# Kernel optimization log

Hardware: AMD Instinct MI355X
Metric: run time of the kernel (lower is better)

The kernel has to match this reference:

```python
import jax, jax.numpy as jnp
import numpy as np

B, T, H, W = 4, 32, 160, 320
NF, FPF = 8, 8          # num_filters, features_per_filter
SPEED_DIM = 8           # speed_embedding output width
U = 64                  # internal LTC neurons (wiring units)
S = NF * FPF + SPEED_DIM  # 72 sensory inputs
M = 1                   # motor (output) neurons
ODE_UNFOLDS = 6
EPS = 1e-8


def setup_inputs() -> dict:
    key = jax.random.key(0)
    k = jax.random.split(key, 20)
    f32 = jnp.float32
    sp = (H // 8) * (W // 8)  # spatial size per filter after 3 stride-2 convs = 800
    d = {}
    d["input_sequence"] = jax.random.normal(k[0], (B, T, 3, H, W), f32)
    d["speed_sequence"] = jax.random.uniform(k[1], (B, T, 1), f32)
    # conv head params
    d["conv1_w"] = jax.random.normal(k[2], (16, 3, 5, 5), f32) * 0.05
    d["conv1_b"] = jnp.zeros((16,), f32)
    d["conv2_w"] = jax.random.normal(k[3], (32, 16, 5, 5), f32) * 0.05
    d["conv2_b"] = jnp.zeros((32,), f32)
    d["conv3_w"] = jax.random.normal(k[4], (NF, 32, 5, 5), f32) * 0.05
    d["conv3_b"] = jnp.zeros((NF,), f32)
    d["head_w"] = jax.random.normal(k[5], (NF, sp, FPF), f32) * 0.02  # per-filter Linear
    d["head_b"] = jnp.zeros((NF, FPF), f32)
    # speed embedding MLP (Dropout is identity at inference)
    d["se_w1"] = jax.random.normal(k[6], (1, 16), f32) * 0.5
    d["se_b1"] = jnp.zeros((16,), f32)
    d["se_w2"] = jax.random.normal(k[7], (16, SPEED_DIM), f32) * 0.3
    d["se_b2"] = jnp.zeros((SPEED_DIM,), f32)
    # LTC cell params (ncps-style init ranges)
    d["input_w"] = jnp.ones((S,), f32)
    d["input_b"] = jnp.zeros((S,), f32)
    d["gleak"] = jax.random.uniform(k[8], (U,), f32, 0.001, 1.0)
    d["vleak"] = jax.random.uniform(k[9], (U,), f32, -0.2, 0.2)
    d["cm"] = jax.random.uniform(k[10], (U,), f32, 0.4, 0.6)
    d["sigma"] = jax.random.uniform(k[11], (U, U), f32, 3.0, 8.0)
    d["mu"] = jax.random.uniform(k[12], (U, U), f32, 0.3, 0.8)
    d["w_syn"] = jax.random.uniform(k[13], (U, U), f32, 0.001, 1.0)
    d["erev"] = jnp.asarray(jax.random.bernoulli(k[14], 0.5, (U, U)), f32) * 2.0 - 1.0
    d["sensory_sigma"] = jax.random.uniform(k[15], (S, U), f32, 3.0, 8.0)
    d["sensory_mu"] = jax.random.uniform(k[16], (S, U), f32, 0.3, 0.8)
    d["sensory_w"] = jax.random.uniform(k[17], (S, U), f32, 0.001, 1.0)
    d["sensory_erev"] = jnp.asarray(jax.random.bernoulli(k[18], 0.5, (S, U)), f32) * 2.0 - 1.0
    d["output_w"] = jnp.ones((M,), f32)
    d["output_b"] = jnp.zeros((M,), f32)
    return d


def _conv(x, w, b, stride):
    y = jax.lax.conv_general_dilated(
        x, w, (stride, stride), [(2, 2), (2, 2)],
        dimension_numbers=("NCHW", "OIHW", "NCHW"))
    return jax.nn.relu(y + b[None, :, None, None])


def reference(input_sequence, speed_sequence, conv1_w, conv1_b, conv2_w, conv2_b,
              conv3_w, conv3_b, head_w, head_b, se_w1, se_b1, se_w2, se_b2,
              input_w, input_b, gleak, vleak, cm, sigma, mu, w_syn, erev,
              sensory_sigma, sensory_mu, sensory_w, sensory_erev, output_w, output_b):
    Bv, Tv = input_sequence.shape[:2]
    # ---- conv head over all frames at once ----
    x = input_sequence.reshape(Bv * Tv, 3, H, W)
    x = _conv(x, conv1_w, conv1_b, 2)
    x = _conv(x, conv2_w, conv2_b, 2)
    x = _conv(x, conv3_w, conv3_b, 2)          # [N, NF, H/8, W/8]
    x = x.reshape(Bv * Tv, NF, -1)             # [N, NF, 800]
    feats = jnp.einsum("nfp,fpk->nfk", x, head_w) + head_b  # per-filter Linear
    feats = feats.reshape(Bv, Tv, NF * FPF)    # [B, T, 64]
    # global-std normalization (torch .std() uses ddof=1)
    feats = feats / (jnp.std(feats, ddof=1) + 1e-5)
    # ---- speed embedding (vectorized over B,T) ----
    s = speed_sequence[..., :1]                # [B, T, 1]
    emb = jnp.tanh(jax.nn.relu(s @ se_w1 + se_b1) @ se_w2 + se_b2)  # [B, T, 8]
    xs = jnp.concatenate([feats, emb], axis=-1)   # [B, T, S]
    xs = jnp.swapaxes(xs, 0, 1)                   # [T, B, S]
    cm_t = cm * ODE_UNFOLDS  # cm / (elapsed_time / ode_unfolds), elapsed_time = 1.0

    def step(v, x_t):
        inp = x_t * input_w + input_b  # affine input mapping, [B, S]
        s_act = sensory_w * jax.nn.sigmoid((inp[:, :, None] - sensory_mu) * sensory_sigma)  # [B,S,U]
        w_num_s = jnp.sum(s_act * sensory_erev, axis=1)
        w_den_s = jnp.sum(s_act, axis=1)
        for _ in range(ODE_UNFOLDS):  # semi-implicit Euler unfolds
            w_act = w_syn * jax.nn.sigmoid((v[:, :, None] - mu) * sigma)  # [B,U,U]
            w_num = jnp.sum(w_act * erev, axis=1) + w_num_s
            w_den = jnp.sum(w_act, axis=1) + w_den_s
            v = (cm_t * v + gleak * vleak + w_num) / (cm_t + gleak + w_den + EPS)
        out = v[:, :M] * output_w + output_b  # affine output mapping on motor neurons
        return v, (out, v)

    v0 = jnp.zeros((Bv, U), feats.dtype)
    v_last, (outs, hs) = jax.lax.scan(step, v0, xs)
    readout = jnp.swapaxes(outs, 0, 1)  # [B, T, M]
    all_h = jnp.swapaxes(hs, 0, 1)      # [B, T, U]
    return readout, v_last, all_h
```

## Files before the change

### kernel.cpp

```cpp
#include <hip/hip_runtime.h>
#include <math.h>

#define BB 4
#define TT 32
#define NF 8
#define FPF 8
#define SDIM 8
#define UU 64
#define SS 72
#define UNFOLDS 6

typedef short short8 __attribute__((ext_vector_type(8)));
typedef float f32x4 __attribute__((ext_vector_type(4)));
union Frag { uint4 u; short8 s; };

__device__ __forceinline__ float fast_sigmoid(float x) {
    float e = exp2f(-1.44269504f * x);
    return __builtin_amdgcn_rcpf(1.0f + e);
}

__device__ __forceinline__ ushort f2b(float f) {
    union { float f; uint u; } a;
    a.f = f;
    uint u = a.u;
    return (ushort)((u + 0x7FFFu + ((u >> 16) & 1u)) >> 16);
}

__device__ __forceinline__ float bcast_lane(float v, int lane) {
    return __uint_as_float(__builtin_amdgcn_readlane(__float_as_uint(v), lane));
}

__device__ __forceinline__ void cvt_body(const float* __restrict__ in,
                                         ushort* __restrict__ outp, int idx) {
    int x = idx % 320;
    int r = idx / 320;
    int y = r % 160;
    int n = r / 160;
    const float* base = in + ((size_t)n * 3 * 160 + y) * 320 + x;
    float c0 = base[0];
    float c1 = base[160 * 320];
    float c2 = base[2 * 160 * 320];
    uint2 pk;
    pk.x = (uint)f2b(c0) | ((uint)f2b(c1) << 16);
    pk.y = (uint)f2b(c2);
    *(uint2*)(outp + ((size_t)((n * 164 + y + 2) * 328) + (x + 2)) * 4) = pk;
}

template <int HP, int WP, int H, int W, int CH>
__device__ __forceinline__ void halo_body(ushort* __restrict__ buf, int bid) {
    constexpr int TOPBOT = 2 * WP;
    constexpr int SIDE = WP - W;
    constexpr int NH = 2 * TOPBOT + H * SIDE;
    int idx = bid * 256 + threadIdx.x;
    if (idx >= 128 * NH) return;
    int n = idx / NH;
    int h = idx - n * NH;
    int y, x;
    if (h < TOPBOT) {
        y = h / WP;
        x = h % WP;
    } else if (h < 2 * TOPBOT) {
        int hh = h - TOPBOT;
        y = H + 2 + hh / WP;
        x = hh % WP;
    } else {
        int hh = h - 2 * TOPBOT;
        y = 2 + hh / SIDE;
        int xi = hh % SIDE;
        x = (xi < 2) ? xi : (W + xi);
    }
    ushort* p = buf + (((size_t)n * HP + y) * WP + x) * CH;
    if constexpr (CH == 4) {
        *(uint2*)p = make_uint2(0u, 0u);
    } else {
        uint4 z = make_uint4(0u, 0u, 0u, 0u);
#pragma unroll
        for (int i = 0; i < CH / 8; i++) *(uint4*)(p + i * 8) = z;
    }
}

__device__ __forceinline__ uint4 pack8(const ushort v[8]) {
    uint4 u;
    u.x = (uint)v[0] | ((uint)v[1] << 16);
    u.y = (uint)v[2] | ((uint)v[3] << 16);
    u.z = (uint)v[4] | ((uint)v[5] << 16);
    u.w = (uint)v[6] | ((uint)v[7] << 16);
    return u;
}

__device__ __forceinline__ void wswz1_body(const float* __restrict__ w, uint4* __restrict__ o,
                                           int i) {
    int lane = i & 63, s = i >> 6;
    int oc = lane & 15, q = lane >> 4;
    ushort v[8];
#pragma unroll
    for (int j = 0; j < 8; j++) {
        int k = q * 8 + j;
        int kx = k >> 2, c = k & 3;
        float f = (kx < 5 && c < 3) ? w[((oc * 3 + c) * 5 + s) * 5 + kx] : 0.f;
        v[j] = f2b(f);
    }
    o[i] = pack8(v);
}
__device__ __forceinline__ void wswz2_body(const float* __restrict__ w, uint4* __restrict__ o,
                                           int i) {
    int lane = i & 63;
    int ct = (i >> 6) & 1;
    int s = i >> 7;
    int ky = s / 3, kxp = s % 3;
    int oc = ct * 16 + (lane & 15);
    int q = lane >> 4, h = q >> 1;
    int kx = 2 * kxp + h;
    ushort v[8];
#pragma unroll
    for (int j = 0; j < 8; j++) {
        int ch = (q & 1) * 8 + j;
        float f = (kx < 5) ? w[((oc * 16 + ch) * 5 + ky) * 5 + kx] : 0.f;
        v[j] = f2b(f);
    }
    o[i] = pack8(v);
}
__device__ __forceinline__ void wswz3_body(const float* __restrict__ w, uint4* __restrict__ o,
                                           int i) {
    int lane = i & 63, s = i >> 6;
    int ky = s / 5, kx = s % 5;
    int oc = lane & 15, q = lane >> 4;
    ushort v[8];
#pragma unroll
    for (int j = 0; j < 8; j++) {
        int ch = q * 8 + j;
        float f = (oc < 8) ? w[((oc * 32 + ch) * 5 + ky) * 5 + kx] : 0.f;
        v[j] = f2b(f);
    }
    o[i] = pack8(v);
}

__global__ __launch_bounds__(256) void prep_kernel(
    const float* __restrict__ in_seq, ushort* __restrict__ inp1, ushort* __restrict__ c1out,
    ushort* __restrict__ c2out, const float* __restrict__ c1w, const float* __restrict__ c2w,
    const float* __restrict__ c3w, uint4* __restrict__ wz1, uint4* __restrict__ wz2,
    uint4* __restrict__ wz3) {
    int bid = blockIdx.x;
    if (bid < 25600) {
        cvt_body(in_seq, inp1, bid * 256 + threadIdx.x);
    } else if (bid < 25600 + 2032) {
        int hb = bid - 25600;
        if (hb < 1296)
            halo_body<164, 328, 160, 320, 4>(inp1, hb);
        else if (hb < 1296 + 488)
            halo_body<84, 164, 80, 160, 16>(c1out, hb - 1296);
        else
            halo_body<44, 84, 40, 80, 32>(c2out, hb - 1784);
    } else {
        int i = (bid - 27632) * 256 + threadIdx.x;
        if (i < 320)
            wswz1_body(c1w, wz1, i);
        else if (i < 2240)
            wswz2_body(c2w, wz2, i - 320);
        else
            wswz3_body(c3w, wz3, i - 2240);
    }
}

__global__ __launch_bounds__(256) void conv1_mfma(const ushort* __restrict__ inp,
                                                  const uint4* __restrict__ wswz,
                                                  const float* __restrict__ bias,
                                                  ushort* __restrict__ outp) {
    const int lane = threadIdx.x & 63;
    const int wid = threadIdx.x >> 6;
    const int col = lane & 15, q = lane >> 4;

    Frag A[5];
#pragma unroll
    for (int s = 0; s < 5; s++) A[s].u = wswz[s * 64 + lane];
    float b0 = bias[q * 4 + 0], b1 = bias[q * 4 + 1], b2 = bias[q * 4 + 2], b3 = bias[q * 4 + 3];

    int gw = blockIdx.x * 4 + wid;
#pragma unroll
    for (int t = 0; t < 4; t++) {
        int p0 = gw * 64 + t * 16;
        int n = p0 / 12800;
        int rem = p0 - n * 12800;
        int oy = rem / 160;
        int ox0 = rem - oy * 160;
        int ox = ox0 + col;
        uint e0 = ((uint)(n * 164 + oy * 2) * 328u + (uint)(ox * 2 + 2 * q)) * 4u;
        f32x4 acc = {0.f, 0.f, 0.f, 0.f};
#pragma unroll
        for (int s = 0; s < 5; s++) {
            Frag B;
            B.u = *(const uint4*)(inp + e0 + (uint)s * (328u * 4u));
            acc = __builtin_amdgcn_mfma_f32_16x16x32_bf16(A[s].s, B.s, acc, 0, 0, 0);
        }
        uint oe = ((uint)(n * 84 + oy + 2) * 164u + (uint)(ox + 2)) * 16u + q * 4u;
        uint2 pk;
        pk.x = (uint)f2b(fmaxf(acc[0] + b0, 0.f)) | ((uint)f2b(fmaxf(acc[1] + b1, 0.f)) << 16);
        pk.y = (uint)f2b(fmaxf(acc[2] + b2, 0.f)) | ((uint)f2b(fmaxf(acc[3] + b3, 0.f)) << 16);
        *(uint2*)(outp + oe) = pk;
    }
}

__global__ __launch_bounds__(256) void conv2_mfma(const ushort* __restrict__ inp,
                                                  const uint4* __restrict__ wswz,
                                                  const float* __restrict__ bias,
                                                  ushort* __restrict__ outp) {
    const int lane = threadIdx.x & 63;
    const int wid = threadIdx.x >> 6;
    const int col = lane & 15, q = lane >> 4;
    const int h = q >> 1, chh = q & 1;

    int gw = blockIdx.x * 4 + wid;
    uint eb[4];
#pragma unroll
    for (int t = 0; t < 4; t++) {
        int p0 = gw * 64 + t * 16;
        int n = p0 / 3200;
        int rem = p0 - n * 3200;
        int oy = rem / 80;
        int ox0 = rem - oy * 80;
        eb[t] = ((uint)(n * 84 + oy * 2) * 164u + (uint)((ox0 + col) * 2 + h)) * 16u + chh * 8u;
    }
    f32x4 acc[4][2];
#pragma unroll
    for (int t = 0; t < 4; t++) {
        acc[t][0] = {0.f, 0.f, 0.f, 0.f};
        acc[t][1] = {0.f, 0.f, 0.f, 0.f};
    }
#pragma unroll
    for (int s = 0; s < 15; s++) {
        const int ky = s / 3, kxp = s % 3;
        Frag A0, A1;
        A0.u = wswz[(s * 2 + 0) * 64 + lane];
        A1.u = wswz[(s * 2 + 1) * 64 + lane];
        const uint d = (uint)ky * (164u * 16u) + (uint)kxp * 32u;
#pragma unroll
        for (int t = 0; t < 4; t++) {
            Frag B;
            B.u = *(const uint4*)(inp + eb[t] + d);
            acc[t][0] = __builtin_amdgcn_mfma_f32_16x16x32_bf16(A0.s, B.s, acc[t][0], 0, 0, 0);
            acc[t][1] = __builtin_amdgcn_mfma_f32_16x16x32_bf16(A1.s, B.s, acc[t][1], 0, 0, 0);
        }
    }
    float ba[2][4];
#pragma unroll
    for (int c = 0; c < 2; c++)
#pragma unroll
        for (int r = 0; r < 4; r++) ba[c][r] = bias[c * 16 + q * 4 + r];
#pragma unroll
    for (int t = 0; t < 4; t++) {
        int p0 = gw * 64 + t * 16;
        int n = p0 / 3200;
        int rem = p0 - n * 3200;
        int oy = rem / 80;
        int ox0 = rem - oy * 80;
        int ox = ox0 + col;
        uint oe = ((uint)(n * 44 + oy + 2) * 84u + (uint)(ox + 2)) * 32u;
#pragma unroll
        for (int c = 0; c < 2; c++) {
            uint2 pk;
            pk.x = (uint)f2b(fmaxf(acc[t][c][0] + ba[c][0], 0.f)) |
                   ((uint)f2b(fmaxf(acc[t][c][1] + ba[c][1], 0.f)) << 16);
            pk.y = (uint)f2b(fmaxf(acc[t][c][2] + ba[c][2], 0.f)) |
                   ((uint)f2b(fmaxf(acc[t][c][3] + ba[c][3], 0.f)) << 16);
            *(uint2*)(outp + oe + (uint)c * 16u + (uint)q * 4u) = pk;
        }
    }
}

__global__ __launch_bounds__(256) void conv3_mfma(const ushort* __restrict__ inp,
                                                  const uint4* __restrict__ wswz,
                                                  const float* __restrict__ bias,
                                                  float* __restrict__ outp) {
    const int lane = threadIdx.x & 63;
    const int wid = threadIdx.x >> 6;
    const int col = lane & 15, q = lane >> 4;

    int gw = blockIdx.x * 4 + wid;
    uint eb[4];
#pragma unroll
    for (int t = 0; t < 4; t++) {
        int p0 = gw * 64 + t * 16;
        int n = p0 / 800;
        int pix = p0 - n * 800 + col;
        int oy = pix / 40;
        int ox = pix - oy * 40;
        eb[t] = ((uint)(n * 44 + oy * 2) * 84u + (uint)(ox * 2)) * 32u + q * 8u;
    }
    f32x4 acc[4];
#pragma unroll
    for (int t = 0; t < 4; t++) acc[t] = {0.f, 0.f, 0.f, 0.f};
#pragma unroll
    for (int s = 0; s < 25; s++) {
        const int ky = s / 5, kx = s % 5;
        Frag A;
        A.u = wswz[s * 64 + lane];
        const uint d = ((uint)ky * 84u + (uint)kx) * 32u;
#pragma unroll
        for (int t = 0; t < 4; t++) {
            Frag B;
            B.u = *(const uint4*)(inp + eb[t] + d);
            acc[t] = __builtin_amdgcn_mfma_f32_16x16x32_bf16(A.s, B.s, acc[t], 0, 0, 0);
        }
    }
    if (q < 2) {
        float b0 = bias[q * 4 + 0], b1 = bias[q * 4 + 1];
        float b2 = bias[q * 4 + 2], b3 = bias[q * 4 + 3];
#pragma unroll
        for (int t = 0; t < 4; t++) {
            int p0 = gw * 64 + t * 16;
            int n = p0 / 800;
            int p = p0 - n * 800 + col;
            float4 v;
            v.x = fmaxf(acc[t][0] + b0, 0.f);
            v.y = fmaxf(acc[t][1] + b1, 0.f);
            v.z = fmaxf(acc[t][2] + b2, 0.f);
            v.w = fmaxf(acc[t][3] + b3, 0.f);
            *(float4*)(outp + ((size_t)n * 800 + p) * 8 + q * 4) = v;
        }
    }
}

__global__ __launch_bounds__(256) void head_kernel(const float* __restrict__ x,
                                                   const float* __restrict__ hw,
                                                   const float* __restrict__ hb,
                                                   float* __restrict__ feats) {
    __shared__ float part[4][64];
    int n = blockIdx.x;
    int tid = threadIdx.x;
    int lane = tid & 63;
    int c = tid >> 6;
    int f = lane >> 3;
    int k = lane & 7;
    const float* xb = x + (size_t)n * 800 * 8 + f;
    const float* wb = hw + ((size_t)f * 800) * FPF + k;
    float acc = 0.0f;
    for (int p = c * 200; p < c * 200 + 200; p++)
        acc = fmaf(xb[(size_t)p * 8], wb[(size_t)p * FPF], acc);
    part[c][lane] = acc;
    __syncthreads();
    if (c == 0)
        feats[n * 64 + lane] = part[0][lane] + part[1][lane] + part[2][lane] + part[3][lane] +
                               hb[lane];
}

__global__ __launch_bounds__(1024) void stats_kernel(const float* __restrict__ feats,
                                                     float* __restrict__ invstd) {
    __shared__ float2 red[1024];
    int tid = threadIdx.x;
    float s = 0.0f, q = 0.0f;
    for (int i = tid; i < 8192; i += 1024) {
        float x = feats[i];
        s += x;
        q += x * x;
    }
    red[tid] = make_float2(s, q);
    __syncthreads();
    for (int off = 512; off > 0; off >>= 1) {
        if (tid < off) {
            float2 o = red[tid + off];
            float2 m = red[tid];
            red[tid] = make_float2(m.x + o.x, m.y + o.y);
        }
        __syncthreads();
    }
    if (tid == 0) {
        float mean = red[0].x / 8192.0f;
        float var = fmaxf((red[0].y - 8192.0f * mean * mean) / 8191.0f, 0.0f);
        invstd[0] = 1.0f / (sqrtf(var) + 1e-5f);
    }
}

__global__ __launch_bounds__(64) void sensory_kernel(
    const float* __restrict__ feats, const float* __restrict__ speed,
    const float* __restrict__ sew1, const float* __restrict__ seb1,
    const float* __restrict__ sew2, const float* __restrict__ seb2,
    const float* __restrict__ invstd, const float* __restrict__ inw,
    const float* __restrict__ inb, const float* __restrict__ ssig,
    const float* __restrict__ smu, const float* __restrict__ sw,
    const float* __restrict__ serev, float* __restrict__ wns, float* __restrict__ wds) {
    int bid = blockIdx.x;
    int t = bid >> 2;
    int b = bid & 3;
    int u = threadIdx.x;
    int n = b * TT + t;
    float inv = invstd[0];

    float sp = speed[n];
    float h[16];
#pragma unroll
    for (int j = 0; j < 16; j++) h[j] = fmaxf(fmaf(sp, sew1[j], seb1[j]), 0.0f);
    float embv[SDIM];
#pragma unroll
    for (int k = 0; k < SDIM; k++) {
        float a = seb2[k];
#pragma unroll
        for (int j = 0; j < 16; j++) a = fmaf(h[j], sew2[j * SDIM + k], a);
        embv[k] = tanhf(a);
    }

    float num = 0.0f, den = 0.0f;
#pragma unroll 4
    for (int ss = 0; ss < 64; ss++) {
        float xsv = feats[n * 64 + ss] * inv;
        float inp = fmaf(xsv, inw[ss], inb[ss]);
        int idx = ss * UU + u;
        float x = (inp - smu[idx]) * ssig[idx];
        float act = sw[idx] * fast_sigmoid(x);
        num = fmaf(act, serev[idx], num);
        den += act;
    }
#pragma unroll
    for (int ss = 64; ss < SS; ss++) {
        float inp = fmaf(embv[ss - 64], inw[ss], inb[ss]);
        int idx = ss * UU + u;
        float x = (inp - smu[idx]) * ssig[idx];
        float act = sw[idx] * fast_sigmoid(x);
        num = fmaf(act, serev[idx], num);
        den += act;
    }
    wns[bid * UU + u] = num;
    wds[bid * UU + u] = den;
}

__global__ __launch_bounds__(512, 1) void scan_kernel(
    const float* __restrict__ wns, const float* __restrict__ wds,
    const float* __restrict__ gleak, const float* __restrict__ vleak,
    const float* __restrict__ cm, const float* __restrict__ sigma,
    const float* __restrict__ mu, const float* __restrict__ wsyn,
    const float* __restrict__ erev, const float* __restrict__ outw,
    const float* __restrict__ outb, float* __restrict__ dout) {
    int b = blockIdx.x;
    int tid = threadIdx.x;
    int u = tid & 63;
    int pc_s = __builtin_amdgcn_readfirstlane(tid >> 6);

    __shared__ float2 pbuf[2][8][64];

    float sA[8], sB[8], wer[8], w_[8];
#pragma unroll
    for (int i = 0; i < 8; i++) {
        int idx = (pc_s * 8 + i) * UU + u;
        float sg = sigma[idx];
        sA[i] = -1.44269504f * sg;
        sB[i] = -sA[i] * mu[idx];
        w_[i] = wsyn[idx];
        wer[i] = w_[i] * erev[idx];
    }
#pragma unroll
    for (int i = 0; i < 8; i++) {
        asm volatile("" : "+v"(sA[i]), "+v"(sB[i]), "+v"(wer[i]), "+v"(w_[i]));
    }
    float cmt = cm[u] * (float)UNFOLDS;
    float gl = gleak[u];
    float glvl = gl * vleak[u];
    float ow = outw[0], ob = outb[0];
    float v = 0.0f;
    int par = 0;

    float num_s = wns[(0 * BB + b) * UU + u];
    float den_s = wds[(0 * BB + b) * UU + u];
    for (int t = 0; t < TT; t++) {
        float nns = 0.f, nds = 0.f;
        if (t + 1 < TT) {
            nns = wns[((t + 1) * BB + b) * UU + u];
            nds = wds[((t + 1) * BB + b) * UU + u];
        }
#pragma unroll
        for (int k = 0; k < UNFOLDS; k++) {
            float num = 0.0f, den = 0.0f;
#pragma unroll
            for (int i = 0; i < 8; i++) {
                float vi = bcast_lane(v, pc_s * 8 + i);
                float e = exp2f(fmaf(vi, sA[i], sB[i]));
                float r = __builtin_amdgcn_rcpf(1.0f + e);
                num = fmaf(wer[i], r, num);
                den = fmaf(w_[i], r, den);
            }
            pbuf[par][pc_s][u] = make_float2(num, den);
            __builtin_amdgcn_sched_barrier(0);
            asm volatile("s_waitcnt lgkmcnt(0)" ::: "memory");
            __builtin_amdgcn_s_barrier();
            asm volatile("" ::: "memory");
            __builtin_amdgcn_sched_barrier(0);
            float nn = num_s, dd = den_s;
#pragma unroll
            for (int j = 0; j < 8; j++) {
                float2 p = pbuf[par][j][u];
                nn += p.x;
                dd += p.y;
            }
            float denom = cmt + gl + dd + 1e-8f;
            v = (fmaf(cmt, v, glvl) + nn) * __builtin_amdgcn_rcpf(denom);
            par ^= 1;
        }
        if (pc_s == 0) {
            dout[384 + (b * TT + t) * UU + u] = v;
            if (u == 0) dout[b * TT + t] = fmaf(v, ow, ob);
            if (t == TT - 1) dout[128 + b * UU + u] = v;
        }
        num_s = nns;
        den_s = nds;
    }
}

extern "C" void kernel_launch(void* const* d_in, const int* in_sizes, int n_in,
                              void* d_out, int out_size, void* d_ws, size_t ws_size,
                              hipStream_t stream) {
    const float* in_seq = (const float*)d_in[0];
    const float* speed = (const float*)d_in[1];
    const float* c1w = (const float*)d_in[2];
    const float* c1b = (const float*)d_in[3];
    const float* c2w = (const float*)d_in[4];
    const float* c2b = (const float*)d_in[5];
    const float* c3w = (const float*)d_in[6];
    const float* c3b = (const float*)d_in[7];
    const float* hw = (const float*)d_in[8];
    const float* hb = (const float*)d_in[9];
    const float* sew1 = (const float*)d_in[10];
    const float* seb1 = (const float*)d_in[11];
    const float* sew2 = (const float*)d_in[12];
    const float* seb2 = (const float*)d_in[13];
    const float* inw = (const float*)d_in[14];
    const float* inb = (const float*)d_in[15];
    const float* gleak = (const float*)d_in[16];
    const float* vleak = (const float*)d_in[17];
    const float* cm = (const float*)d_in[18];
    const float* sigma = (const float*)d_in[19];
    const float* mu = (const float*)d_in[20];
    const float* wsyn = (const float*)d_in[21];
    const float* erev = (const float*)d_in[22];
    const float* ssig = (const float*)d_in[23];
    const float* smu = (const float*)d_in[24];
    const float* sw = (const float*)d_in[25];
    const float* serev = (const float*)d_in[26];
    const float* outw = (const float*)d_in[27];
    const float* outb = (const float*)d_in[28];

    char* ws = (char*)d_ws;
    float* out = (float*)d_out;

    size_t off = 0;
    auto alloc = [&](size_t bytes) {
        size_t o = off;
        off += (bytes + 255) & ~(size_t)255;
        return o;
    };
    ushort* inp1 = (ushort*)(ws + alloc((size_t)128 * 164 * 328 * 4 * 2));
    ushort* c1out = (ushort*)(ws + alloc((size_t)128 * 84 * 164 * 16 * 2));
    ushort* c2out = (ushort*)(ws + alloc((size_t)128 * 44 * 84 * 32 * 2));
    float* c3out = (float*)(ws + alloc((size_t)128 * 800 * 8 * 4));
    float* feats = (float*)(ws + alloc(8192 * 4));
    float* invstd = (float*)(ws + alloc(64));
    float* wns = (float*)(ws + alloc(8192 * 4));
    float* wds = (float*)(ws + alloc(8192 * 4));
    uint4* wz1 = (uint4*)(ws + alloc(5 * 64 * 16));
    uint4* wz2 = (uint4*)(ws + alloc(30 * 64 * 16));
    uint4* wz3 = (uint4*)(ws + alloc(25 * 64 * 16));

    prep_kernel<<<27647, 256, 0, stream>>>(in_seq, inp1, c1out, c2out, c1w, c2w, c3w, wz1,
                                           wz2, wz3);

    conv1_mfma<<<6400, 256, 0, stream>>>(inp1, wz1, c1b, c1out);
    conv2_mfma<<<1600, 256, 0, stream>>>(c1out, wz2, c2b, c2out);
    conv3_mfma<<<400, 256, 0, stream>>>(c2out, wz3, c3b, c3out);

    head_kernel<<<128, 256, 0, stream>>>(c3out, hw, hb, feats);

    stats_kernel<<<1, 1024, 0, stream>>>(feats, invstd);

    sensory_kernel<<<128, 64, 0, stream>>>(feats, speed, sew1, seb1, sew2, seb2, invstd, inw,
                                           inb, ssig, smu, sw, serev, wns, wds);

    scan_kernel<<<BB, 512, 0, stream>>>(wns, wds, gleak, vleak, cm, sigma, mu, wsyn, erev,
                                        outw, outb, out);
}
```

Measured before the change: 253.4 us.

## Fuse fp32-to-bf16 input conversion and padding into conv1 MFMA loads

Removes the separate conversion pass that wrote a padded bf16 NHWC copy of the input image, and the halo zeroing for that buffer. conv1 now reads the fp32 NCHW input directly, clamps indices, masks out-of-bounds taps and packs bf16 fragments in registers. This saves a full write and re-read of a large intermediate buffer. In exchange conv1 issues six scalar, strided fp32 loads per tap across three channel planes instead of one vector load, and repeats the conversion for overlapping windows.

```diff
diff --git a/kernel.cpp b/kernel.cpp
--- a/kernel.cpp
+++ b/kernel.cpp
@@ -26,24 +26,12 @@
     return (ushort)((u + 0x7FFFu + ((u >> 16) & 1u)) >> 16);
 }
 
+__device__ __forceinline__ uint pk_bf16(float lo, float hi) {
+    return (uint)f2b(lo) | ((uint)f2b(hi) << 16);
+}
+
 __device__ __forceinline__ float bcast_lane(float v, int lane) {
     return __uint_as_float(__builtin_amdgcn_readlane(__float_as_uint(v), lane));
-}
-
-__device__ __forceinline__ void cvt_body(const float* __restrict__ in,
-                                         ushort* __restrict__ outp, int idx) {
-    int x = idx % 320;
-    int r = idx / 320;
-    int y = r % 160;
-    int n = r / 160;
-    const float* base = in + ((size_t)n * 3 * 160 + y) * 320 + x;
-    float c0 = base[0];
-    float c1 = base[160 * 320];
-    float c2 = base[2 * 160 * 320];
-    uint2 pk;
-    pk.x = (uint)f2b(c0) | ((uint)f2b(c1) << 16);
-    pk.y = (uint)f2b(c2);
-    *(uint2*)(outp + ((size_t)((n * 164 + y + 2) * 328) + (x + 2)) * 4) = pk;
 }
 
 template <int HP, int WP, int H, int W, int CH>
@@ -70,13 +58,9 @@
         x = (xi < 2) ? xi : (W + xi);
     }
     ushort* p = buf + (((size_t)n * HP + y) * WP + x) * CH;
-    if constexpr (CH == 4) {
-        *(uint2*)p = make_uint2(0u, 0u);
-    } else {
-        uint4 z = make_uint4(0u, 0u, 0u, 0u);
-#pragma unroll
-        for (int i = 0; i < CH / 8; i++) *(uint4*)(p + i * 8) = z;
-    }
+    uint4 z = make_uint4(0u, 0u, 0u, 0u);
+#pragma unroll
+    for (int i = 0; i < CH / 8; i++) *(uint4*)(p + i * 8) = z;
 }
 
 __device__ __forceinline__ uint4 pack8(const ushort v[8]) {
@@ -136,23 +120,16 @@
 }
 
 __global__ __launch_bounds__(256) void prep_kernel(
-    const float* __restrict__ in_seq, ushort* __restrict__ inp1, ushort* __restrict__ c1out,
-    ushort* __restrict__ c2out, const float* __restrict__ c1w, const float* __restrict__ c2w,
-    const float* __restrict__ c3w, uint4* __restrict__ wz1, uint4* __restrict__ wz2,
-    uint4* __restrict__ wz3) {
+    ushort* __restrict__ c1out, ushort* __restrict__ c2out, const float* __restrict__ c1w,
+    const float* __restrict__ c2w, const float* __restrict__ c3w, uint4* __restrict__ wz1,
+    uint4* __restrict__ wz2, uint4* __restrict__ wz3) {
     int bid = blockIdx.x;
-    if (bid < 25600) {
-        cvt_body(in_seq, inp1, bid * 256 + threadIdx.x);
-    } else if (bid < 25600 + 2032) {
-        int hb = bid - 25600;
-        if (hb < 1296)
-            halo_body<164, 328, 160, 320, 4>(inp1, hb);
-        else if (hb < 1296 + 488)
-            halo_body<84, 164, 80, 160, 16>(c1out, hb - 1296);
-        else
-            halo_body<44, 84, 40, 80, 32>(c2out, hb - 1784);
+    if (bid < 488) {
+        halo_body<84, 164, 80, 160, 16>(c1out, bid);
+    } else if (bid < 736) {
+        halo_body<44, 84, 40, 80, 32>(c2out, bid - 488);
     } else {
-        int i = (bid - 27632) * 256 + threadIdx.x;
+        int i = (bid - 736) * 256 + threadIdx.x;
         if (i < 320)
             wswz1_body(c1w, wz1, i);
         else if (i < 2240)
@@ -162,10 +139,10 @@
     }
 }
 
-__global__ __launch_bounds__(256) void conv1_mfma(const ushort* __restrict__ inp,
-                                                  const uint4* __restrict__ wswz,
-                                                  const float* __restrict__ bias,
-                                                  ushort* __restrict__ outp) {
+__global__ __launch_bounds__(256) void conv1_fused(const float* __restrict__ in,
+                                                   const uint4* __restrict__ wswz,
+                                                   const float* __restrict__ bias,
+                                                   ushort* __restrict__ outp) {
     const int lane = threadIdx.x & 63;
     const int wid = threadIdx.x >> 6;
     const int col = lane & 15, q = lane >> 4;
@@ -184,12 +161,34 @@
         int oy = rem / 160;
         int ox0 = rem - oy * 160;
         int ox = ox0 + col;
-        uint e0 = ((uint)(n * 164 + oy * 2) * 328u + (uint)(ox * 2 + 2 * q)) * 4u;
+        int ix0 = ox * 2 + 2 * q - 2;
+        int ixc0 = min(max(ix0, 0), 319);
+        int ixc1 = min(max(ix0 + 1, 0), 319);
+        bool vx0 = (ix0 >= 0) & (ix0 < 320) & (q < 3);
+        bool vx1 = (ix0 + 1 >= 0) & (ix0 + 1 < 320) & (q < 2);
+        const float* inb = in + (size_t)n * 3 * 160 * 320;
+
         f32x4 acc = {0.f, 0.f, 0.f, 0.f};
 #pragma unroll
         for (int s = 0; s < 5; s++) {
+            int iy = oy * 2 + s - 2;
+            bool vy = (iy >= 0) & (iy < 160);
+            const float* row = inb + (size_t)(vy ? iy : 0) * 320;
+            bool v0 = vy & vx0, v1 = vy & vx1;
+            float c00 = row[ixc0], c01 = row[ixc1];
+            float c10 = row[51200 + ixc0], c11 = row[51200 + ixc1];
+            float c20 = row[102400 + ixc0], c21 = row[102400 + ixc1];
+            c00 = v0 ? c00 : 0.f;
+            c10 = v0 ? c10 : 0.f;
+            c20 = v0 ? c20 : 0.f;
+            c01 = v1 ? c01 : 0.f;
+            c11 = v1 ? c11 : 0.f;
+            c21 = v1 ? c21 : 0.f;
             Frag B;
-            B.u = *(const uint4*)(inp + e0 + (uint)s * (328u * 4u));
+            B.u.x = pk_bf16(c00, c10);
+            B.u.y = (uint)f2b(c20);
+            B.u.z = pk_bf16(c01, c11);
+            B.u.w = (uint)f2b(c21);
             acc = __builtin_amdgcn_mfma_f32_16x16x32_bf16(A[s].s, B.s, acc, 0, 0, 0);
         }
         uint oe = ((uint)(n * 84 + oy + 2) * 164u + (uint)(ox + 2)) * 16u + q * 4u;
@@ -545,7 +544,6 @@
         off += (bytes + 255) & ~(size_t)255;
         return o;
     };
-    ushort* inp1 = (ushort*)(ws + alloc((size_t)128 * 164 * 328 * 4 * 2));
     ushort* c1out = (ushort*)(ws + alloc((size_t)128 * 84 * 164 * 16 * 2));
     ushort* c2out = (ushort*)(ws + alloc((size_t)128 * 44 * 84 * 32 * 2));
     float* c3out = (float*)(ws + alloc((size_t)128 * 800 * 8 * 4));
@@ -557,10 +555,10 @@
     uint4* wz2 = (uint4*)(ws + alloc(30 * 64 * 16));
     uint4* wz3 = (uint4*)(ws + alloc(25 * 64 * 16));
 
-    prep_kernel<<<27647, 256, 0, stream>>>(in_seq, inp1, c1out, c2out, c1w, c2w, c3w, wz1,
-                                           wz2, wz3);
-
-    conv1_mfma<<<6400, 256, 0, stream>>>(inp1, wz1, c1b, c1out);
+    prep_kernel<<<751, 256, 0, stream>>>(c1out, c2out, c1w, c2w, c3w, wz1, wz2, wz3);
+
+    conv1_fused<<<6400, 256, 0, stream>>>(in_seq, wz1, c1b, c1out);
+
     conv2_mfma<<<1600, 256, 0, stream>>>(c1out, wz2, c2b, c2out);
     conv3_mfma<<<400, 256, 0, stream>>>(c2out, wz3, c3b, c3out);
 
```

Result: slower. 303.5 us (+19.8%).
